# Optimization experiments

Hardware: AMD Instinct MI355X
Metric: run time of the kernel (lower is better)

## Reference

```python
import jax, jax.numpy as jnp
import numpy as np

N = 100000   # nodes
E = 800000   # edges (avg degree ~8)
G = 64       # graphs in batch
F_IN = 64
H = 128
C = 4


def setup_inputs() -> dict:
    key = jax.random.key(0)
    ks = jax.random.split(key, 14)
    def w(k, fin, fout):
        return jax.random.normal(k, (fin, fout), dtype=jnp.float32) * (1.0 / np.sqrt(fin))
    inp = {
        "x": jax.random.normal(ks[0], (N, F_IN), dtype=jnp.float32),
        "W1": w(ks[1], F_IN, H), "b1": jnp.zeros((H,), jnp.float32),
        "W2": w(ks[2], H, H),    "b2": jnp.zeros((H,), jnp.float32),
        "W3": w(ks[3], H, H),    "b3": jnp.zeros((H,), jnp.float32),
        "fw1": w(ks[4], H, H),   "fb1": jnp.zeros((H,), jnp.float32),
        "fw2": w(ks[5], H, C),   "fb2": jnp.zeros((C,), jnp.float32),
        "edge_index": jax.random.randint(ks[6], (2, E), 0, N, dtype=jnp.int32),
        "batch": jnp.sort(jax.random.randint(ks[7], (N,), 0, G, dtype=jnp.int32)),
    }
    return inp


def gcn_conv(x, W, b, src, dst):
    """PyG GCNConv: linear transform, add self-loops, symmetric deg^-1/2 norm, scatter-add."""
    h = x @ W                                                    # [N, H]
    deg = jax.ops.segment_sum(jnp.ones((E,), x.dtype), dst, num_segments=N) + 1.0  # self-loop
    dinv = jax.lax.rsqrt(deg)                                    # [N]
    norm = dinv[src] * dinv[dst]                                 # [E]
    agg = jax.ops.segment_sum(h[src] * norm[:, None], dst, num_segments=N)
    agg = agg + h * (dinv * dinv)[:, None]                       # self-loop term (norm = 1/deg)
    return agg + b


def reference(x, W1, b1, W2, b2, W3, b3, fw1, fb1, fw2, fb2, edge_index, batch):
    src, dst = edge_index[0], edge_index[1]
    h = jax.nn.relu(gcn_conv(x, W1, b1, src, dst))
    h = jax.nn.relu(gcn_conv(h, W2, b2, src, dst))
    h = gcn_conv(h, W3, b3, src, dst)
    # global mean pool over graphs
    s = jax.ops.segment_sum(h, batch, num_segments=G)            # [G, H]
    cnt = jax.ops.segment_sum(jnp.ones((N,), h.dtype), batch, num_segments=G)
    pooled = s / jnp.maximum(cnt, 1.0)[:, None]
    z = jax.nn.relu(pooled @ fw1 + fb1)
    return z @ fw2 + fb2                                          # [G, C]
```

## Files before the change

### kernel.cpp

```cpp
#include <hip/hip_runtime.h>

#define N_NODES 100000
#define N_EDGES 800000
#define G_GRAPHS 64
#define F_INPUT 64
#define H_DIM 128
#define C_OUT 4
#define CSR_CAP 32
#define EDGE_BLOCKS (N_EDGES / 256)
#define CONV_BLOCKS ((N_NODES + 255) / 256)
#define WPACK_BLOCKS 20
#define FILL_SEG 4
#define FILL_CHUNKS 250
#define FILL_RANGE (N_NODES / FILL_SEG)
#define FILL_CHUNK (N_EDGES / FILL_CHUNKS)
#define FILL_BLOCKS (FILL_SEG * FILL_CHUNKS)
#define SEG_SPAN (FILL_RANGE * CSR_CAP)

typedef __attribute__((ext_vector_type(8))) short bf16x8;
typedef __attribute__((ext_vector_type(8))) unsigned short u16x8;
typedef __attribute__((ext_vector_type(4))) float f32x4;

__device__ inline unsigned short f2bf(float f) {
    union { float f; unsigned int u; } v; v.f = f;
    unsigned int u = v.u + 0x7FFFu + ((v.u >> 16) & 1u);
    return (unsigned short)(u >> 16);
}
__device__ inline float bf2f(unsigned short b) {
    union { unsigned int u; float f; } v; v.u = ((unsigned int)b) << 16;
    return v.f;
}
__device__ inline float2 unpack_pair(unsigned int u) {
    union { unsigned int u; float f; } a, b;
    a.u = u << 16; b.u = u & 0xFFFF0000u;
    float2 r; r.x = a.f; r.y = b.f; return r;
}
__device__ inline unsigned char f2fp8(float v) {
    int r = __builtin_amdgcn_cvt_pk_fp8_f32(v, 0.0f, 0, false);
    return (unsigned char)(r & 0xFF);
}

__device__ inline void wpack_one(const float* __restrict__ W, unsigned short* __restrict__ hi,
                                 unsigned short* __restrict__ lo, int K, int t)
{
    int lane = t & 63;
    int tile = t >> 6;
    int KS = K / 32;
    int ct = tile / KS, ks = tile % KS;
    int n  = ct * 16 + (lane & 15);
    int k0 = ks * 32 + (lane >> 4) * 8;
    #pragma unroll
    for (int j = 0; j < 8; j++) {
        float w = W[(k0 + j) * H_DIM + n];
        unsigned short h = f2bf(w);
        hi[t * 8 + j] = h;
        lo[t * 8 + j] = f2bf(w - bf2f(h));
    }
}

__global__ __launch_bounds__(256) void hist_kernel(
    const int* __restrict__ dst, int* __restrict__ cnt, int* __restrict__ paddr,
    const float* __restrict__ W1, const float* __restrict__ W2, const float* __restrict__ W3,
    unsigned short* __restrict__ w1hi, unsigned short* __restrict__ w1lo,
    unsigned short* __restrict__ w2hi, unsigned short* __restrict__ w2lo,
    unsigned short* __restrict__ w3hi, unsigned short* __restrict__ w3lo)
{
    int b = blockIdx.x;
    if (b < EDGE_BLOCKS) {
        int e = b * 256 + threadIdx.x;
        int d = dst[e];
        int sl = atomicAdd(&cnt[d], 1);
        paddr[e] = (sl < CSR_CAP) ? d * CSR_CAP + sl : -1;
        return;
    }
    b -= EDGE_BLOCKS;
    int t = b * 256 + threadIdx.x;
    if (t < 1024)       wpack_one(W1, w1hi, w1lo, F_INPUT, t);
    else if (t < 3072)  wpack_one(W2, w2hi, w2lo, H_DIM, t - 1024);
    else                wpack_one(W3, w3hi, w3lo, H_DIM, t - 3072);
}

__global__ __launch_bounds__(256) void prep_kernel(
    const int* __restrict__ paddr, const int* __restrict__ src,
    int* __restrict__ csr,
    const int* __restrict__ cnti, const float4* __restrict__ x4,
    float* __restrict__ dinv, unsigned int* __restrict__ xb_u,
    unsigned int* __restrict__ p1z, unsigned int* __restrict__ p3z)
{
    int b = blockIdx.x;
    if (b < FILL_BLOCKS) {
        const int r   = b & (FILL_SEG - 1);
        const int m   = b >> 2;
        const int plo = r * SEG_SPAN;
        const int phi = plo + SEG_SPAN;
        const int e0  = m * FILL_CHUNK;
        for (int e = e0 + threadIdx.x; e < e0 + FILL_CHUNK; e += 256) {
            int pa = paddr[e];
            if (pa >= plo && pa < phi)
                csr[pa] = src[e];
        }
        return;
    }
    b -= FILL_BLOCKS;
    __shared__ float dl[256];
    int i = b * 256 + threadIdx.x;
    float dv = 0.0f;
    if (i < N_NODES) {
        int c  = cnti[i];
        int dc = min(c, CSR_CAP);
        dv = rsqrtf((float)c + 1.0f);
        dinv[i] = dv;
        int pad = (dc + 7) & ~7;
        for (int s2 = dc; s2 < pad; s2++)
            csr[(size_t)i * CSR_CAP + s2] = N_NODES;
    } else if (i == N_NODES) {
        for (int c = 0; c < 32; c++) {
            xb_u[(size_t)N_NODES * 32 + c] = 0u;
            p1z [(size_t)N_NODES * 32 + c] = 0u;
            p3z [(size_t)N_NODES * 32 + c] = 0u;
        }
    }
    dl[threadIdx.x] = dv;
    __syncthreads();
    const int row_base = b * 256;
    for (int c = threadIdx.x; c < 256 * 16; c += 256) {
        int r = c >> 4;
        int row = row_base + r;
        if (row < N_NODES) {
            float d2 = dl[r];
            float4 v = x4[(size_t)row * 16 + (c & 15)];
            size_t o = ((size_t)row * 16 + (c & 15)) * 2;
            xb_u[o + 0] = (unsigned int)f2bf(v.x * d2) | ((unsigned int)f2bf(v.y * d2) << 16);
            xb_u[o + 1] = (unsigned int)f2bf(v.z * d2) | ((unsigned int)f2bf(v.w * d2) << 16);
        }
    }
}

__global__ __launch_bounds__(256) void gather1_kernel(
    const unsigned int* __restrict__ xb_u, const int* __restrict__ cnti,
    const int* __restrict__ csr, const float* __restrict__ dinv,
    unsigned int* __restrict__ outb)
{
    int idx = blockIdx.x * 256 + threadIdx.x;
    int i  = idx >> 5;
    int f2 = idx & 31;
    int dc = min(cnti[i], CSR_CAP);
    int beg  = i * CSR_CAP;
    int end8 = beg + ((dc + 7) & ~7);
    float2 acc = unpack_pair(xb_u[(size_t)i * 32 + f2]);
    for (int e = beg; e < end8; e += 8) {
        int4 c0 = *(const int4*)(csr + e);
        int4 c1 = *(const int4*)(csr + e + 4);
        float2 v0 = unpack_pair(xb_u[(size_t)c0.x * 32 + f2]);
        float2 v1 = unpack_pair(xb_u[(size_t)c0.y * 32 + f2]);
        float2 v2 = unpack_pair(xb_u[(size_t)c0.z * 32 + f2]);
        float2 v3 = unpack_pair(xb_u[(size_t)c0.w * 32 + f2]);
        float2 v4 = unpack_pair(xb_u[(size_t)c1.x * 32 + f2]);
        float2 v5 = unpack_pair(xb_u[(size_t)c1.y * 32 + f2]);
        float2 v6 = unpack_pair(xb_u[(size_t)c1.z * 32 + f2]);
        float2 v7 = unpack_pair(xb_u[(size_t)c1.w * 32 + f2]);
        acc.x += ((v0.x + v1.x) + (v2.x + v3.x)) + ((v4.x + v5.x) + (v6.x + v7.x));
        acc.y += ((v0.y + v1.y) + (v2.y + v3.y)) + ((v4.y + v5.y) + (v6.y + v7.y));
    }
    float dv = dinv[i];
    outb[idx] = (unsigned int)f2bf(acc.x * dv) | ((unsigned int)f2bf(acc.y * dv) << 16);
}

__device__ inline void acc_u2(uint2 w, float* __restrict__ a) {
    auto l0 = __builtin_amdgcn_cvt_pk_f32_fp8(w.x, false);
    auto h0 = __builtin_amdgcn_cvt_pk_f32_fp8(w.x, true);
    auto l1 = __builtin_amdgcn_cvt_pk_f32_fp8(w.y, false);
    auto h1 = __builtin_amdgcn_cvt_pk_f32_fp8(w.y, true);
    a[0] += l0[0]; a[1] += l0[1]; a[2] += h0[0]; a[3] += h0[1];
    a[4] += l1[0]; a[5] += l1[1]; a[6] += h1[0]; a[7] += h1[1];
}
__device__ inline void gather_fp8_u2(
    const uint2* __restrict__ base, const int* __restrict__ csr,
    int i, int beg, int end8, float* __restrict__ a)
{
    acc_u2(base[(size_t)i * 16], a);
    for (int e = beg; e < end8; e += 8) {
        int4 c0 = *(const int4*)(csr + e);
        int4 c1 = *(const int4*)(csr + e + 4);
        uint2 w0 = base[(size_t)c0.x * 16];
        uint2 w1 = base[(size_t)c0.y * 16];
        uint2 w2 = base[(size_t)c0.z * 16];
        uint2 w3 = base[(size_t)c0.w * 16];
        uint2 w4 = base[(size_t)c1.x * 16];
        uint2 w5 = base[(size_t)c1.y * 16];
        uint2 w6 = base[(size_t)c1.z * 16];
        uint2 w7 = base[(size_t)c1.w * 16];
        acc_u2(w0, a); acc_u2(w1, a); acc_u2(w2, a); acc_u2(w3, a);
        acc_u2(w4, a); acc_u2(w5, a); acc_u2(w6, a); acc_u2(w7, a);
    }
}

__global__ __launch_bounds__(256) void gemm_g2f_kernel(
    const uint2* __restrict__ hs8, const int* __restrict__ cnti,
    const int* __restrict__ csr, const float* __restrict__ dinv,
    const unsigned short* __restrict__ whi, const unsigned short* __restrict__ wlo,
    const float* __restrict__ bias, unsigned char* __restrict__ out8)
{
    constexpr int KS = 4;
    __shared__ unsigned short As[16 * 128];
    uint4* As4 = (uint4*)As;
    const int tid  = threadIdx.x;
    const int row0 = blockIdx.x * 16;

    {
        int r  = tid >> 4;
        int f8 = tid & 15;
        int gr = row0 + r;
        int dc = min(cnti[gr], CSR_CAP);
        int beg  = gr * CSR_CAP;
        int end8 = beg + ((dc + 7) & ~7);
        float a[8] = {0, 0, 0, 0, 0, 0, 0, 0};
        gather_fp8_u2(hs8 + f8, csr, gr, beg, end8, a);
        float dv = dinv[gr];
        float4 b0 = *(const float4*)(bias + f8 * 8);
        float4 b1 = *(const float4*)(bias + f8 * 8 + 4);
        float v0 = fmaxf(a[0] * dv + b0.x, 0.0f);
        float v1 = fmaxf(a[1] * dv + b0.y, 0.0f);
        float v2 = fmaxf(a[2] * dv + b0.z, 0.0f);
        float v3 = fmaxf(a[3] * dv + b0.w, 0.0f);
        float v4 = fmaxf(a[4] * dv + b1.x, 0.0f);
        float v5 = fmaxf(a[5] * dv + b1.y, 0.0f);
        float v6 = fmaxf(a[6] * dv + b1.z, 0.0f);
        float v7 = fmaxf(a[7] * dv + b1.w, 0.0f);
        uint4 o;
        o.x = (unsigned int)f2bf(v0) | ((unsigned int)f2bf(v1) << 16);
        o.y = (unsigned int)f2bf(v2) | ((unsigned int)f2bf(v3) << 16);
        o.z = (unsigned int)f2bf(v4) | ((unsigned int)f2bf(v5) << 16);
        o.w = (unsigned int)f2bf(v6) | ((unsigned int)f2bf(v7) << 16);
        As4[(f8 >> 2) * 64 + (f8 & 3) * 16 + r] = o;
    }
    __syncthreads();

    const int w = tid >> 6, lane = tid & 63;
    const int quad = lane >> 4, l16 = lane & 15;
    const int ct0 = w * 2;

    f32x4 acc[2];
    acc[0] = (f32x4)(0.0f);
    acc[1] = (f32x4)(0.0f);
    #pragma unroll
    for (int ks = 0; ks < KS; ks++) {
        bf16x8 a0 = *(const bf16x8*)(As + (ks * 64 + lane) * 8);
        bf16x8 bh[2], bl[2];
        #pragma unroll
        for (int c = 0; c < 2; c++) {
            bh[c] = *(const bf16x8*)(whi + ((size_t)((ct0 + c) * KS + ks) * 64 + lane) * 8);
            bl[c] = *(const bf16x8*)(wlo + ((size_t)((ct0 + c) * KS + ks) * 64 + lane) * 8);
        }
        #pragma unroll
        for (int c = 0; c < 2; c++) {
            acc[c] = __builtin_amdgcn_mfma_f32_16x16x32_bf16(a0, bh[c], acc[c], 0, 0, 0);
            acc[c] = __builtin_amdgcn_mfma_f32_16x16x32_bf16(a0, bl[c], acc[c], 0, 0, 0);
        }
    }
    #pragma unroll
    for (int reg = 0; reg < 4; reg++) {
        int row = row0 + quad * 4 + reg;
        float dvr = dinv[row];
        #pragma unroll
        for (int c = 0; c < 2; c++)
            out8[(size_t)row * H_DIM + (ct0 + c) * 16 + l16] = f2fp8(acc[c][reg] * dvr);
    }
}

__global__ __launch_bounds__(256) void gather3_kernel(
    const uint2* __restrict__ hs8, const int* __restrict__ cnti,
    const int* __restrict__ csr, const float* __restrict__ dinv,
    const float* __restrict__ bias, uint4* __restrict__ outb)
{
    int idx = blockIdx.x * 256 + threadIdx.x;
    int i  = idx >> 4;
    int f8 = idx & 15;
    int dc = min(cnti[i], CSR_CAP);
    int beg  = i * CSR_CAP;
    int end8 = beg + ((dc + 7) & ~7);
    float a[8] = {0, 0, 0, 0, 0, 0, 0, 0};
    gather_fp8_u2(hs8 + f8, csr, i, beg, end8, a);
    float dv = dinv[i];
    float4 b0 = *(const float4*)(bias + f8 * 8);
    float4 b1 = *(const float4*)(bias + f8 * 8 + 4);
    uint4 o;
    o.x = (unsigned int)f2bf(a[0] * dv + b0.x) | ((unsigned int)f2bf(a[1] * dv + b0.y) << 16);
    o.y = (unsigned int)f2bf(a[2] * dv + b0.z) | ((unsigned int)f2bf(a[3] * dv + b0.w) << 16);
    o.z = (unsigned int)f2bf(a[4] * dv + b1.x) | ((unsigned int)f2bf(a[5] * dv + b1.y) << 16);
    o.w = (unsigned int)f2bf(a[6] * dv + b1.z) | ((unsigned int)f2bf(a[7] * dv + b1.w) << 16);
    outb[(size_t)i * 16 + f8] = o;
}

template <int K, bool BIAS_RELU, bool IN_FP8>
__global__ __launch_bounds__(256) void mfma_gemm_kernel(
    const void* __restrict__ inv, const unsigned short* __restrict__ whi,
    const unsigned short* __restrict__ wlo, const float* __restrict__ dinv,
    const float* __restrict__ bias, unsigned char* __restrict__ out8)
{
    constexpr int KS = K / 32;
    __shared__ unsigned short As[128 * K];

    const int tid  = threadIdx.x;
    const int row0 = blockIdx.x * 128;

    const int CH = 128 * K / 8;
    for (int c = tid; c < CH; c += 256) {
        int mt   = c / (KS * 64);
        int rest = c % (KS * 64);
        int ks   = rest / 64;
        int ln   = rest % 64;
        int r    = mt * 16 + (ln & 15);
        int k    = ks * 32 + (ln >> 4) * 8;
        int gr   = row0 + r; if (gr >= N_NODES) gr = N_NODES - 1;
        if constexpr (IN_FP8) {
            const unsigned char* in8 = (const unsigned char*)inv;
            uint2 t = *(const uint2*)(in8 + (size_t)gr * K + k);
            auto f0 = __builtin_amdgcn_cvt_pk_f32_fp8(t.x, false);
            auto f1 = __builtin_amdgcn_cvt_pk_f32_fp8(t.x, true);
            auto f2 = __builtin_amdgcn_cvt_pk_f32_fp8(t.y, false);
            auto f3 = __builtin_amdgcn_cvt_pk_f32_fp8(t.y, true);
            unsigned int* Au = (unsigned int*)(As + c * 8);
            Au[0] = (unsigned int)f2bf(f0[0]) | ((unsigned int)f2bf(f0[1]) << 16);
            Au[1] = (unsigned int)f2bf(f1[0]) | ((unsigned int)f2bf(f1[1]) << 16);
            Au[2] = (unsigned int)f2bf(f2[0]) | ((unsigned int)f2bf(f2[1]) << 16);
            Au[3] = (unsigned int)f2bf(f3[0]) | ((unsigned int)f2bf(f3[1]) << 16);
        } else {
            const unsigned short* in16 = (const unsigned short*)inv;
            *(u16x8*)(As + c * 8) = *(const u16x8*)(in16 + (size_t)gr * K + k);
        }
    }
    __syncthreads();

    const int w = tid >> 6, lane = tid & 63;
    const int quad = lane >> 4, l16 = lane & 15;

    f32x4 acc[2][8];
    #pragma unroll
    for (int rt = 0; rt < 2; rt++)
        #pragma unroll
        for (int ct = 0; ct < 8; ct++) acc[rt][ct] = (f32x4)(0.0f);

    #pragma unroll
    for (int ks = 0; ks < KS; ks++) {
        bf16x8 a0 = *(const bf16x8*)(As + (((w * 2 + 0) * KS + ks) * 64 + lane) * 8);
        bf16x8 a1 = *(const bf16x8*)(As + (((w * 2 + 1) * KS + ks) * 64 + lane) * 8);
        bf16x8 bh[8], bl[8];
        #pragma unroll
        for (int ct = 0; ct < 8; ct++) {
            bh[ct] = *(const bf16x8*)(whi + ((size_t)(ct * KS + ks) * 64 + lane) * 8);
            bl[ct] = *(const bf16x8*)(wlo + ((size_t)(ct * KS + ks) * 64 + lane) * 8);
        }
        #pragma unroll
        for (int ct = 0; ct < 8; ct++) {
            acc[0][ct] = __builtin_amdgcn_mfma_f32_16x16x32_bf16(a0, bh[ct], acc[0][ct], 0, 0, 0);
            acc[0][ct] = __builtin_amdgcn_mfma_f32_16x16x32_bf16(a0, bl[ct], acc[0][ct], 0, 0, 0);
            acc[1][ct] = __builtin_amdgcn_mfma_f32_16x16x32_bf16(a1, bh[ct], acc[1][ct], 0, 0, 0);
            acc[1][ct] = __builtin_amdgcn_mfma_f32_16x16x32_bf16(a1, bl[ct], acc[1][ct], 0, 0, 0);
        }
    }

    float bv[8];
    if (BIAS_RELU) {
        #pragma unroll
        for (int ct = 0; ct < 8; ct++) bv[ct] = bias[ct * 16 + l16];
    }

    #pragma unroll
    for (int rt = 0; rt < 2; rt++) {
        #pragma unroll
        for (int reg = 0; reg < 4; reg++) {
            int row = row0 + w * 32 + rt * 16 + quad * 4 + reg;
            if (row < N_NODES) {
                float dv = BIAS_RELU ? 0.0f : dinv[row];
                #pragma unroll
                for (int ct = 0; ct < 8; ct++) {
                    float val;
                    if (BIAS_RELU) val = fmaxf(acc[rt][ct][reg] + bv[ct], 0.0f);
                    else           val = acc[rt][ct][reg] * dv;
                    out8[(size_t)row * H_DIM + ct * 16 + l16] = f2fp8(val);
                }
            }
        }
    }
}

__global__ __launch_bounds__(128) void pool_kernel(
    const unsigned short* __restrict__ A, const int* __restrict__ batch,
    float* __restrict__ s, float* __restrict__ cnt)
{
    const int RPB = 32;
    int row0 = blockIdx.x * RPB;
    int f = threadIdx.x;
    int g0 = batch[row0];
    int g1 = batch[row0 + RPB - 1];
    if (g0 == g1) {
        float acc = 0.0f;
        #pragma unroll
        for (int r = 0; r < RPB; r++)
            acc += bf2f(A[(size_t)(row0 + r) * H_DIM + f]);
        unsafeAtomicAdd(&s[g0 * H_DIM + f], acc);
        if (f == 0) unsafeAtomicAdd(&cnt[g0], (float)RPB);
    } else {
        float acc = 0.0f;
        int cur = g0, c = 0;
        for (int r = 0; r < RPB; r++) {
            int g = batch[row0 + r];
            if (g != cur) {
                unsafeAtomicAdd(&s[cur * H_DIM + f], acc);
                if (f == 0) unsafeAtomicAdd(&cnt[cur], (float)c);
                cur = g; acc = 0.0f; c = 0;
            }
            acc += bf2f(A[(size_t)(row0 + r) * H_DIM + f]);
            c++;
        }
        unsafeAtomicAdd(&s[cur * H_DIM + f], acc);
        if (f == 0) unsafeAtomicAdd(&cnt[cur], (float)c);
    }
}

__global__ __launch_bounds__(128) void mlp_kernel(
    const float* __restrict__ s, const float* __restrict__ cnt,
    const float* __restrict__ fw1, const float* __restrict__ fb1,
    const float* __restrict__ fw2, const float* __restrict__ fb2,
    float* __restrict__ out)
{
    __shared__ float p[H_DIM];
    __shared__ float z[H_DIM];
    int g = blockIdx.x;
    int f = threadIdx.x;
    float c = fmaxf(cnt[g], 1.0f);
    p[f] = s[g * H_DIM + f] / c;
    __syncthreads();
    float acc = fb1[f];
    for (int k = 0; k < H_DIM; k++) acc = fmaf(p[k], fw1[k * H_DIM + f], acc);
    z[f] = fmaxf(acc, 0.0f);
    __syncthreads();
    if (f < C_OUT) {
        float o = fb2[f];
        for (int k = 0; k < H_DIM; k++) o = fmaf(z[k], fw2[k * C_OUT + f], o);
        out[g * C_OUT + f] = o;
    }
}

extern "C" void kernel_launch(void* const* d_in, const int* in_sizes, int n_in,
                              void* d_out, int out_size, void* d_ws, size_t ws_size,
                              hipStream_t stream)
{
    const float* x   = (const float*)d_in[0];
    const float* W1  = (const float*)d_in[1];
    const float* b1  = (const float*)d_in[2];
    const float* W2  = (const float*)d_in[3];
    const float* b2  = (const float*)d_in[4];
    const float* W3  = (const float*)d_in[5];
    const float* b3  = (const float*)d_in[6];
    const float* fw1 = (const float*)d_in[7];
    const float* fb1 = (const float*)d_in[8];
    const float* fw2 = (const float*)d_in[9];
    const float* fb2 = (const float*)d_in[10];
    const int*   ei  = (const int*)d_in[11];
    const int*   bat = (const int*)d_in[12];
    const int* esrc = ei;
    const int* edst = ei + N_EDGES;
    float* out = (float*)d_out;

    char* ws = (char*)d_ws;
    unsigned short* xb   = (unsigned short*)ws; ws += (size_t)(N_NODES + 1) * F_INPUT * 2;
    unsigned short* aggA = (unsigned short*)ws; ws += (size_t)N_NODES * F_INPUT * 2;
    unsigned short* aggB = (unsigned short*)ws; ws += (size_t)N_NODES * H_DIM * 2;
    unsigned char*  p0 = (unsigned char*)ws;  ws += (size_t)(N_NODES + 1) * H_DIM;
    unsigned char*  p1 = (unsigned char*)ws;  ws += (size_t)(N_NODES + 1) * H_DIM;
    unsigned char*  p3 = (unsigned char*)ws;  ws += (size_t)(N_NODES + 1) * H_DIM;
    unsigned short* w1hi = (unsigned short*)ws; ws += H_DIM * F_INPUT * 2;
    unsigned short* w1lo = (unsigned short*)ws; ws += H_DIM * F_INPUT * 2;
    unsigned short* w2hi = (unsigned short*)ws; ws += H_DIM * H_DIM * 2;
    unsigned short* w2lo = (unsigned short*)ws; ws += H_DIM * H_DIM * 2;
    unsigned short* w3hi = (unsigned short*)ws; ws += H_DIM * H_DIM * 2;
    unsigned short* w3lo = (unsigned short*)ws; ws += H_DIM * H_DIM * 2;
    float* dinv = (float*)ws;  ws += N_NODES * 4;
    int* paddr  = (int*)ws;    ws += (size_t)N_EDGES * 4;
    int* csr    = (int*)ws;    ws += (size_t)N_NODES * CSR_CAP * 4;
    int*   cnti = (int*)ws;    ws += N_NODES * 4;
    float* s    = (float*)ws;  ws += G_GRAPHS * H_DIM * 4;
    float* cnt  = (float*)ws;  ws += G_GRAPHS * 4;

    hipMemsetAsync(cnti, 0, (N_NODES + G_GRAPHS * H_DIM + G_GRAPHS) * sizeof(int), stream);

    hist_kernel<<<EDGE_BLOCKS + WPACK_BLOCKS, 256, 0, stream>>>(
        edst, cnti, paddr, W1, W2, W3, w1hi, w1lo, w2hi, w2lo, w3hi, w3lo);
    prep_kernel<<<FILL_BLOCKS + CONV_BLOCKS, 256, 0, stream>>>(
        paddr, esrc, csr, cnti, (const float4*)x, dinv, (unsigned int*)xb,
        (unsigned int*)p1, (unsigned int*)p3);

    const int gemm_grid = (N_NODES + 127) / 128;

    gather1_kernel<<<(N_NODES * 32) / 256, 256, 0, stream>>>(
        (const unsigned int*)xb, cnti, csr, dinv, (unsigned int*)aggA);
    mfma_gemm_kernel<64, true, false><<<gemm_grid, 256, 0, stream>>>(
        aggA, w1hi, w1lo, dinv, b1, p0);
    mfma_gemm_kernel<128, false, true><<<gemm_grid, 256, 0, stream>>>(
        p0, w2hi, w2lo, dinv, nullptr, p1);
    gemm_g2f_kernel<<<N_NODES / 16, 256, 0, stream>>>(
        (const uint2*)p1, cnti, csr, dinv, w3hi, w3lo, b2, p3);
    gather3_kernel<<<(N_NODES * 16) / 256, 256, 0, stream>>>(
        (const uint2*)p3, cnti, csr, dinv, b3, (uint4*)aggB);

    pool_kernel<<<N_NODES / 32, 128, 0, stream>>>(aggB, bat, s, cnt);
    mlp_kernel<<<G_GRAPHS, 128, 0, stream>>>(s, cnt, fw1, fb1, fw2, fb2, out);
}
```

Measured before the change: 302.8 us.

## Fuse layer-1 neighbor gather into the MFMA GEMM kernel

Replaces the separate layer-1 gather kernel and 64-wide GEMM with one kernel in which each 16-row block gathers and sums bf16 neighbor features into shared memory and then runs a bf16 hi/lo MFMA against W1, applying bias, ReLU and fp8 output. This removes the aggA intermediate write and re-read and one kernel launch. In exchange each block covers only 16 rows, so W1 fragments are reloaded far more often and each thread now gathers 8-byte chunks instead of 4-byte ones.

```diff
diff --git a/kernel.cpp b/kernel.cpp
--- a/kernel.cpp
+++ b/kernel.cpp
@@ -136,34 +136,92 @@
     }
 }
 
-__global__ __launch_bounds__(256) void gather1_kernel(
-    const unsigned int* __restrict__ xb_u, const int* __restrict__ cnti,
+__global__ __launch_bounds__(256) void gemm_g1f_kernel(
+    const uint2* __restrict__ xb2, const int* __restrict__ cnti,
     const int* __restrict__ csr, const float* __restrict__ dinv,
-    unsigned int* __restrict__ outb)
-{
-    int idx = blockIdx.x * 256 + threadIdx.x;
-    int i  = idx >> 5;
-    int f2 = idx & 31;
-    int dc = min(cnti[i], CSR_CAP);
-    int beg  = i * CSR_CAP;
-    int end8 = beg + ((dc + 7) & ~7);
-    float2 acc = unpack_pair(xb_u[(size_t)i * 32 + f2]);
-    for (int e = beg; e < end8; e += 8) {
-        int4 c0 = *(const int4*)(csr + e);
-        int4 c1 = *(const int4*)(csr + e + 4);
-        float2 v0 = unpack_pair(xb_u[(size_t)c0.x * 32 + f2]);
-        float2 v1 = unpack_pair(xb_u[(size_t)c0.y * 32 + f2]);
-        float2 v2 = unpack_pair(xb_u[(size_t)c0.z * 32 + f2]);
-        float2 v3 = unpack_pair(xb_u[(size_t)c0.w * 32 + f2]);
-        float2 v4 = unpack_pair(xb_u[(size_t)c1.x * 32 + f2]);
-        float2 v5 = unpack_pair(xb_u[(size_t)c1.y * 32 + f2]);
-        float2 v6 = unpack_pair(xb_u[(size_t)c1.z * 32 + f2]);
-        float2 v7 = unpack_pair(xb_u[(size_t)c1.w * 32 + f2]);
-        acc.x += ((v0.x + v1.x) + (v2.x + v3.x)) + ((v4.x + v5.x) + (v6.x + v7.x));
-        acc.y += ((v0.y + v1.y) + (v2.y + v3.y)) + ((v4.y + v5.y) + (v6.y + v7.y));
-    }
-    float dv = dinv[i];
-    outb[idx] = (unsigned int)f2bf(acc.x * dv) | ((unsigned int)f2bf(acc.y * dv) << 16);
+    const unsigned short* __restrict__ whi, const unsigned short* __restrict__ wlo,
+    const float* __restrict__ bias, unsigned char* __restrict__ out8)
+{
+    constexpr int KS = 2;
+    __shared__ unsigned short As[16 * 64];
+    uint2* As2 = (uint2*)As;
+    const int tid  = threadIdx.x;
+    const int row0 = blockIdx.x * 16;
+
+    {
+        int r  = tid >> 4;
+        int f8 = tid & 15;
+        int gr = row0 + r;
+        int dc = min(cnti[gr], CSR_CAP);
+        int beg  = gr * CSR_CAP;
+        int end8 = beg + ((dc + 7) & ~7);
+        const uint2* base = xb2 + f8;
+        float a0, a1, a2, a3;
+        {
+            uint2 w = base[(size_t)gr * 16];
+            float2 p0 = unpack_pair(w.x), p1 = unpack_pair(w.y);
+            a0 = p0.x; a1 = p0.y; a2 = p1.x; a3 = p1.y;
+        }
+        for (int e = beg; e < end8; e += 8) {
+            int4 c0 = *(const int4*)(csr + e);
+            int4 c1 = *(const int4*)(csr + e + 4);
+            uint2 w0 = base[(size_t)c0.x * 16];
+            uint2 w1 = base[(size_t)c0.y * 16];
+            uint2 w2 = base[(size_t)c0.z * 16];
+            uint2 w3 = base[(size_t)c0.w * 16];
+            uint2 w4 = base[(size_t)c1.x * 16];
+            uint2 w5 = base[(size_t)c1.y * 16];
+            uint2 w6 = base[(size_t)c1.z * 16];
+            uint2 w7 = base[(size_t)c1.w * 16];
+            #pragma unroll
+            for (uint2 w : {w0, w1, w2, w3, w4, w5, w6, w7}) {
+                float2 p0 = unpack_pair(w.x), p1 = unpack_pair(w.y);
+                a0 += p0.x; a1 += p0.y; a2 += p1.x; a3 += p1.y;
+            }
+        }
+        float dv = dinv[gr];
+        uint2 o;
+        o.x = (unsigned int)f2bf(a0 * dv) | ((unsigned int)f2bf(a1 * dv) << 16);
+        o.y = (unsigned int)f2bf(a2 * dv) | ((unsigned int)f2bf(a3 * dv) << 16);
+        int ks = f8 >> 3, quad = (f8 >> 1) & 3, bb = f8 & 1;
+        As2[((ks * 64 + quad * 16 + r) << 1) | bb] = o;
+    }
+    __syncthreads();
+
+    const int w = tid >> 6, lane = tid & 63;
+    const int quad = lane >> 4, l16 = lane & 15;
+    const int ct0 = w * 2;
+
+    f32x4 acc[2];
+    acc[0] = (f32x4)(0.0f);
+    acc[1] = (f32x4)(0.0f);
+    #pragma unroll
+    for (int ks = 0; ks < KS; ks++) {
+        bf16x8 a0 = *(const bf16x8*)(As + (ks * 64 + lane) * 8);
+        bf16x8 bh[2], bl[2];
+        #pragma unroll
+        for (int c = 0; c < 2; c++) {
+            bh[c] = *(const bf16x8*)(whi + ((size_t)((ct0 + c) * KS + ks) * 64 + lane) * 8);
+            bl[c] = *(const bf16x8*)(wlo + ((size_t)((ct0 + c) * KS + ks) * 64 + lane) * 8);
+        }
+        #pragma unroll
+        for (int c = 0; c < 2; c++) {
+            acc[c] = __builtin_amdgcn_mfma_f32_16x16x32_bf16(a0, bh[c], acc[c], 0, 0, 0);
+            acc[c] = __builtin_amdgcn_mfma_f32_16x16x32_bf16(a0, bl[c], acc[c], 0, 0, 0);
+        }
+    }
+    float bv[2];
+    #pragma unroll
+    for (int c = 0; c < 2; c++) bv[c] = bias[(ct0 + c) * 16 + l16];
+    #pragma unroll
+    for (int reg = 0; reg < 4; reg++) {
+        int row = row0 + quad * 4 + reg;
+        #pragma unroll
+        for (int c = 0; c < 2; c++) {
+            float val = fmaxf(acc[c][reg] + bv[c], 0.0f);
+            out8[(size_t)row * H_DIM + (ct0 + c) * 16 + l16] = f2fp8(val);
+        }
+    }
 }
 
 __device__ inline void acc_u2(uint2 w, float* __restrict__ a) {
@@ -466,7 +524,6 @@
 
     char* ws = (char*)d_ws;
     unsigned short* xb   = (unsigned short*)ws; ws += (size_t)(N_NODES + 1) * F_INPUT * 2;
-    unsigned short* aggA = (unsigned short*)ws; ws += (size_t)N_NODES * F_INPUT * 2;
     unsigned short* aggB = (unsigned short*)ws; ws += (size_t)N_NODES * H_DIM * 2;
     unsigned char*  p0 = (unsigned char*)ws;  ws += (size_t)(N_NODES + 1) * H_DIM;
     unsigned char*  p1 = (unsigned char*)ws;  ws += (size_t)(N_NODES + 1) * H_DIM;
@@ -494,10 +551,8 @@
 
     const int gemm_grid = (N_NODES + 127) / 128;
 
-    gather1_kernel<<<(N_NODES * 32) / 256, 256, 0, stream>>>(
-        (const unsigned int*)xb, cnti, csr, dinv, (unsigned int*)aggA);
-    mfma_gemm_kernel<64, true, false><<<gemm_grid, 256, 0, stream>>>(
-        aggA, w1hi, w1lo, dinv, b1, p0);
+    gemm_g1f_kernel<<<N_NODES / 16, 256, 0, stream>>>(
+        (const uint2*)xb, cnti, csr, dinv, w1hi, w1lo, b1, p0);
     mfma_gemm_kernel<128, false, true><<<gemm_grid, 256, 0, stream>>>(
         p0, w2hi, w2lo, dinv, nullptr, p1);
     gemm_g2f_kernel<<<N_NODES / 16, 256, 0, stream>>>(
```

New measurement: 288.0 us. 1.05x faster.
